# Kernel tuning notes

Measured on AMD Instinct MI355X. Metric: run time of the kernel, lower is better.

Reference implementation:

```python
import jax, jax.numpy as jnp
import numpy as np
import math

DIFF = True   # params['diff'] -> kind='random_walk'
SHIFT = 0.0   # params['shift']
MIN_WINDOW = 10
EPS = 1e-6


def _window_sizes(T):
    ws = []
    cur = math.log10(MIN_WINDOW)
    end = math.log10(T - 1)
    while cur < end:
        w = int(10 ** cur)
        if MIN_WINDOW <= w <= T - 1:
            ws.append(w)
        cur += 0.25
    if T not in ws:
        ws.append(T)
    return sorted(set(ws))


def _hurst_random_walk(x):
    B, T = x.shape
    ws = _window_sizes(T)  # static python list (shapes are static)
    rs_list = []
    for w in ws:
        n = T // w
        seg = x[:, : n * w].reshape(B, n, w)            # (B, n, w)
        d = seg[..., 1:] - seg[..., :-1]                # (B, n, w-1)
        mean_inc = (seg[..., -1] - seg[..., 0]) / (w - 1)
        dev = d - mean_inc[..., None]
        Z = jnp.cumsum(dev, axis=-1)                    # rescaled-range scan
        R = jnp.max(Z, axis=-1) - jnp.min(Z, axis=-1)   # (B, n)
        S = jnp.std(d, axis=-1, ddof=1)                 # unbiased std
        rs_list.append(jnp.mean(R / (S + EPS), axis=-1))
    RS = jnp.stack(rs_list, axis=1)                     # (B, K)
    X = jnp.log10(jnp.asarray(ws, dtype=x.dtype) + EPS) # (K,)
    Y = jnp.log10(RS + EPS)
    Xc = X - jnp.mean(X)
    denom = jnp.sum(Xc * Xc)
    H = jnp.sum((Y - jnp.mean(Y, axis=1, keepdims=True)) * Xc, axis=1) / (denom + EPS)
    H = jnp.where(jnp.isfinite(H), H, jnp.asarray(1.0, x.dtype))
    return H


def setup_inputs() -> dict:
    key = jax.random.key(0)
    x = jax.random.normal(key, (8192, 4096), dtype=jnp.float32)
    return {"x": x}


def reference(x):
    H = _hurst_random_walk(x)
    return (H + SHIFT)[:, None]  # (B, 1)
```

## Files before the change

kernel.cpp:

```cpp
#include <hip/hip_runtime.h>
#include <math.h>
#include <utility>

#define TLEN 4096
#define NW   12
#define BLOCK 256
#define EPSF 1e-6f

typedef float v2f __attribute__((ext_vector_type(2)));

__device__ const float XC_TAB[NW] = {
    -1.3608041f, -1.1303552f, -0.8694424f, -0.6126161f,
    -0.3608041f, -0.1128308f,  0.1388830f,  0.3889322f,
     0.6391959f,  0.8891277f,  1.1391578f,  1.2515558f };
__device__ const float INVN_TAB[NW] = {
    1.0f/409.0f, 1.0f/240.0f, 1.0f/132.0f, 1.0f/73.0f,
    1.0f/40.0f,  1.0f/23.0f,  1.0f/12.0f,  1.0f/7.0f,
    0.25f, 0.5f, 1.0f, 1.0f };
#define INV_DEN 0.11577579f
#define LOG10_2 0.30102999566f

__device__ __forceinline__ float max3f(float a, float b, float c) {
    float r; asm("v_max3_f32 %0, %1, %2, %3" : "=v"(r) : "v"(a), "v"(b), "v"(c)); return r;
}
__device__ __forceinline__ float min3f(float a, float b, float c) {
    float r; asm("v_min3_f32 %0, %1, %2, %3" : "=v"(r) : "v"(a), "v"(b), "v"(c)); return r;
}
__device__ __forceinline__ v2f pk_fma(v2f a, v2f b, v2f c) {
    v2f d; asm("v_pk_fma_f32 %0, %1, %2, %3" : "=v"(d) : "v"(a), "v"(b), "v"(c)); return d;
}
__device__ __forceinline__ v2f pk_add(v2f a, v2f b) {
    v2f d; asm("v_pk_add_f32 %0, %1, %2" : "=v"(d) : "v"(a), "v"(b)); return d;
}

__device__ __forceinline__ float wave_reduce_sum(float v) {
    #pragma unroll
    for (int o = 32; o > 0; o >>= 1) v += __shfl_xor(v, o, 64);
    return v;
}
template<int G>
__device__ __forceinline__ float reduce_leaders(float v) {
    #pragma unroll
    for (int o = G; o < 64; o <<= 1) v += __shfl_xor(v, o, 64);
    return v;
}

template<int FLO, int FHI>
__device__ __forceinline__ float seg_rs2(const float* __restrict__ row,
                                         const float* __restrict__ P4,
                                         int b, int W, float m, float invwm2,
                                         float mx, float mn) {
    float plo = P4[b >> 2];
    if constexpr (FLO > 0) {
        const int k0 = b - FLO;
        #pragma unroll
        for (int t = 0; t < FLO; ++t) {
            float d = row[k0 + t + 1] - row[k0 + t];
            plo = fmaf(d, d, plo);
        }
    }
    const int e = b + W - 1;
    float phi = P4[e >> 2];
    if constexpr (FHI > 0) {
        const int k0 = e - FHI;
        #pragma unroll
        for (int t = 0; t < FHI; ++t) {
            float d = row[k0 + t + 1] - row[k0 + t];
            phi = fmaf(d, d, phi);
        }
    }
    float ss  = phi - plo;
    float var = fmaf(-(float)(W - 1) * m, m, ss) * invwm2;
    float S   = __builtin_amdgcn_sqrtf(fmaxf(var, 0.0f));
    return (mx - mn) * __builtin_amdgcn_rcpf(S + EPSF);
}

template<int LO, int HI, int JB>
__device__ __forceinline__ void chunk_fold(const float4 q, float nm, float& mx, float& mn) {
    if constexpr (LO <= HI) {
        constexpr int NV = HI - LO + 1;
        float v[NV];
        #pragma unroll
        for (int r = 0; r < NV; ++r)
            v[r] = fmaf((float)(JB + LO + r), nm, (&q.x)[LO + r]);
        if constexpr (NV == 1) { mx = fmaxf(mx, v[0]); mn = fminf(mn, v[0]); }
        else if constexpr (NV == 2) { mx = max3f(mx, v[0], v[1]); mn = min3f(mn, v[0], v[1]); }
        else if constexpr (NV == 3) { mx = fmaxf(mx, max3f(v[0], v[1], v[2]));
                                      mn = fminf(mn, min3f(v[0], v[1], v[2])); }
        else { mx = max3f(max3f(mx, v[0], v[1]), v[2], v[3]);
               mn = min3f(min3f(mn, v[0], v[1]), v[2], v[3]); }
    }
}

template<int W, int NSEG, int C>
__device__ __forceinline__ void mchunk_step(const float4* __restrict__ p,
                                            const float (&nm)[NSEG],
                                            float (&mx)[NSEG], float (&mn)[NSEG]) {
    constexpr int E0 = 4 * C;
    constexpr int K0 = E0 / W;
    constexpr int SA = K0 * W;
    constexpr int LOA = (SA == E0) ? 1 : 0;
    constexpr int HIA_ = SA + W - 1 - E0;
    constexpr int HIA = HIA_ < 3 ? HIA_ : 3;
    float4 q = p[C];
    if constexpr (K0 < NSEG)
        chunk_fold<LOA, HIA, E0 - SA>(q, nm[K0], mx[K0], mn[K0]);
    constexpr bool HASB = (K0 + 1 < NSEG) && (SA + W + 1 - E0 <= 3);
    if constexpr (HASB) {
        constexpr int SB = SA + W;
        chunk_fold<SB + 1 - E0, 3, E0 - SB>(q, nm[K0 + 1], mx[K0 + 1], mn[K0 + 1]);
    }
}

template<int W, int NSEG, int... Cs>
__device__ __forceinline__ void mseg_all(const float4* __restrict__ p,
                                         const float (&nm)[NSEG],
                                         float (&mx)[NSEG], float (&mn)[NSEG],
                                         std::integer_sequence<int, Cs...>) {
    (mchunk_step<W, NSEG, Cs>(p, nm, mx, mn), ...);
}

template<int W, int NSEG, int... Ks>
__device__ __forceinline__ float mseg_rs_all(const float* __restrict__ row,
                                             const float* __restrict__ P4, int b,
                                             const float (&m)[NSEG],
                                             const float (&mx)[NSEG], const float (&mn)[NSEG],
                                             std::integer_sequence<int, Ks...>) {
    constexpr float invwm2 = 1.0f / (float)(W - 2);
    float acc = 0.0f;
    ((acc += seg_rs2<(W * Ks) & 3, (W * Ks + W - 1) & 3>(
          row, P4, b + Ks * W, W, m[Ks], invwm2, mx[Ks], mn[Ks])), ...);
    return acc;
}

template<int W, int NSEG>
__device__ __forceinline__ float mseg_task_odd(const float* __restrict__ row,
                                               const float* __restrict__ P4, int b) {
    constexpr int NCH = (W * NSEG + 3) / 4;
    const float4* p = (const float4*)(row + b);
    float nm[NSEG], m[NSEG], mx[NSEG], mn[NSEG];
    #pragma unroll
    for (int k = 0; k < NSEG; ++k) {
        float a0 = row[b + k * W];
        float a1 = row[b + k * W + W - 1];
        m[k] = (a1 - a0) * (1.0f / (float)(W - 1));
        nm[k] = -m[k];
        mx[k] = -INFINITY; mn[k] = INFINITY;
    }
    mseg_all<W, NSEG>(p, nm, mx, mn, std::make_integer_sequence<int, NCH>{});
    return mseg_rs_all<W, NSEG>(row, P4, b, m, mx, mn,
                                std::make_integer_sequence<int, NSEG>{});
}

template<int W, int A, int G>
__device__ __forceinline__ void seg_strided_pk(const float* __restrict__ row, int b, int lane,
                                               float nm, float& mx, float& mn) {
    constexpr int NCH  = (A + W - 1) / 4 + 1;
    constexpr int HIL  = (A + W - 1) & 3;
    constexpr int MAIN_END = (HIL == 3) ? NCH : NCH - 1;
    constexpr int NFULL = MAIN_END - 1;
    constexpr int FULL  = NFULL / G;
    constexpr int REM   = NFULL % G;
    constexpr int NB    = FULL + (REM > 0 ? 1 : 0);
    const float4* p  = (const float4*)(row + (b - A));
    const float4* pl = p + (1 + lane);
    float4 qs[NB > 0 ? NB : 1];
    #pragma unroll
    for (int i = 0; i < FULL; ++i) qs[i] = pl[i * G];
    if constexpr (REM > 0) { if (lane < REM) qs[FULL] = pl[FULL * G]; }
    mx = -INFINITY; mn = INFINITY;
    v2f jc; jc.x = (float)(4 * (1 + lane) - A); jc.y = jc.x + 1.0f;
    const v2f nm2   = {nm, nm};
    const v2f nm2x2 = {nm + nm, nm + nm};
    const v2f step  = {(float)(4 * G), (float)(4 * G)};
    #pragma unroll
    for (int i = 0; i < FULL; ++i) {
        float4 q = qs[i];
        v2f q01 = {q.x, q.y}, q23 = {q.z, q.w};
        v2f t01 = pk_fma(jc, nm2, q01);
        v2f t23 = pk_fma(jc, nm2, pk_add(q23, nm2x2));
        mx = max3f(max3f(mx, t01.x, t01.y), t23.x, t23.y);
        mn = min3f(min3f(mn, t01.x, t01.y), t23.x, t23.y);
        jc = pk_add(jc, step);
    }
    if constexpr (REM > 0) {
        if (lane < REM) {
            float4 q = qs[FULL];
            v2f q01 = {q.x, q.y}, q23 = {q.z, q.w};
            v2f t01 = pk_fma(jc, nm2, q01);
            v2f t23 = pk_fma(jc, nm2, pk_add(q23, nm2x2));
            mx = max3f(max3f(mx, t01.x, t01.y), t23.x, t23.y);
            mn = min3f(min3f(mn, t01.x, t01.y), t23.x, t23.y);
        }
    }
    if constexpr (A < 3) {
        if (lane == 0) chunk_fold<A + 1, 3, -A>(p[0], nm, mx, mn);
    }
    if constexpr (HIL != 3) {
        if (lane == 1) chunk_fold<0, HIL, 4 * (NCH - 1) - A>(p[NCH - 1], nm, mx, mn);
    }
}

template<int W, int A, int G>
__device__ __forceinline__ float group_seg(const float* __restrict__ row,
                                           const float* __restrict__ P4,
                                           int s, int lane) {
    const int b = s * W;
    float a0 = row[b], a1 = row[b + W - 1];
    float m = (a1 - a0) * (1.0f / (float)(W - 1));
    float nm = -m;
    float mx, mn;
    seg_strided_pk<W, A, G>(row, b, lane, nm, mx, mn);
    #pragma unroll
    for (int o = G / 2; o > 0; o >>= 1) {
        mx = fmaxf(mx, __shfl_xor(mx, o, G));
        mn = fminf(mn, __shfl_xor(mn, o, G));
    }
    float r = seg_rs2<A, (A + W - 1) & 3>(
        row, P4, b, W, m, 1.0f / (float)(W - 2), mx, mn);
    return (lane == 0) ? r : 0.0f;
}

__device__ __forceinline__ float w10_seg10(const float (&v)[10], float ss) {
    const float m = (v[9] - v[0]) * (1.0f / 9.0f), nm = -m;
    float x1 = fmaf(1.0f, nm, v[1]);
    float x2 = fmaf(2.0f, nm, v[2]);
    float x3 = fmaf(3.0f, nm, v[3]);
    float x4 = fmaf(4.0f, nm, v[4]);
    float x5 = fmaf(5.0f, nm, v[5]);
    float x6 = fmaf(6.0f, nm, v[6]);
    float x7 = fmaf(7.0f, nm, v[7]);
    float x8 = fmaf(8.0f, nm, v[8]);
    float x9 = fmaf(9.0f, nm, v[9]);
    float mx = max3f(x1, x2, x3);
    mx = max3f(mx, x4, x5); mx = max3f(mx, x6, x7); mx = max3f(mx, x8, x9);
    float mn = min3f(x1, x2, x3);
    mn = min3f(mn, x4, x5); mn = min3f(mn, x6, x7); mn = min3f(mn, x8, x9);
    float var = fmaf(-9.0f * m, m, ss) * 0.125f;
    float S = __builtin_amdgcn_sqrtf(fmaxf(var, 0.0f));
    return (mx - mn) * __builtin_amdgcn_rcpf(S + EPSF);
}

__global__ __launch_bounds__(BLOCK, 7) void hurst_kernel(const float* __restrict__ x,
                                                         float* __restrict__ out) {
    __shared__ __align__(16) float row[TLEN];
    __shared__ __align__(16) float P4[TLEN / 4];
    __shared__ float rs_sum[NW];
    __shared__ float wred[8];
    __shared__ float wredB[24];

    const int tid = threadIdx.x;
    const int r = blockIdx.x;
    const int w = tid >> 6, l = tid & 63;

    const float4* src = (const float4*)(x + (size_t)r * TLEN);
    float4* dst = (float4*)row;
    #pragma unroll
    for (int i = 0; i < TLEN / 4 / BLOCK; ++i)
        dst[tid + i * BLOCK] = src[tid + i * BLOCK];
    if (tid < NW) rs_sum[tid] = 0.0f;
    __syncthreads();

    {
        float lp1 = 0.0f, lp2 = 0.0f, lp3 = 0.0f, lp4 = 0.0f;
        float total = 0.0f;
        float contrib = 0.0f;
        if (tid < 205) {
            const int b = tid * 20;
            const float4* p = (const float4*)(row + b);
            float4 q0 = p[0], q1 = p[1], q2 = p[2];
            float v[12] = {q0.x,q0.y,q0.z,q0.w, q1.x,q1.y,q1.z,q1.w,
                           q2.x,q2.y,q2.z,q2.w};
            float c = 0.0f, s9 = 0.0f;
            #pragma unroll
            for (int j = 0; j < 10; ++j) {
                if (j == 4) lp1 = c;
                if (j == 8) lp2 = c;
                if (j == 9) s9 = c;
                float d = v[j + 1] - v[j];
                c = fmaf(d, d, c);
            }
            {
                float a1[10] = {v[0],v[1],v[2],v[3],v[4],v[5],v[6],v[7],v[8],v[9]};
                contrib = w10_seg10(a1, s9);
            }
            const float s10 = c;
            const float v10 = v[10], v11 = v[11];
            float d10 = v11 - v10;
            c = fmaf(d10, d10, c);
            if (tid < 204) {
                float4 q3 = p[3], q4 = p[4];
                float u[8] = {q3.x,q3.y,q3.z,q3.w, q4.x,q4.y,q4.z,q4.w};
                float vlast = row[b + 20];
                float d11 = u[0] - v11;
                c = fmaf(d11, d11, c);
                lp3 = c;
                float s19 = 0.0f;
                #pragma unroll
                for (int j = 12; j < 20; ++j) {
                    if (j == 16) lp4 = c;
                    if (j == 19) s19 = c;
                    float nxt = (j + 1 < 20) ? u[j - 11] : vlast;
                    float d = nxt - u[j - 12];
                    c = fmaf(d, d, c);
                }
                float a2[10] = {v10, v11, u[0],u[1],u[2],u[3],u[4],u[5],u[6],u[7]};
                contrib += w10_seg10(a2, s19 - s10);
                total = c;
            } else {
                float4 q3 = p[3];
                float d11 = q3.x - v11;
                c = fmaf(d11, d11, c);
                lp3 = c;
                float d12 = q3.y - q3.x; c = fmaf(d12, d12, c);
                float d13 = q3.z - q3.y; c = fmaf(d13, d13, c);
                float d14 = q3.w - q3.z; c = fmaf(d14, d14, c);
                total = c;
            }
        }
        float incl = total;
        #pragma unroll
        for (int o = 1; o < 64; o <<= 1) {
            float u = __shfl_up(incl, o, 64);
            if (l >= o) incl += u;
        }
        if (l == 63) wred[w] = incl;
        float a = wave_reduce_sum(contrib);
        if (l == 0) atomicAdd(&rs_sum[0], a);
        __syncthreads();
        float off = incl - total;
        #pragma unroll
        for (int w2 = 0; w2 < 4; ++w2)
            if (w2 < w) off += wred[w2];
        if (tid < 204) {
            const int h = tid * 5;
            P4[h]     = off;
            P4[h + 1] = off + lp1;
            P4[h + 2] = off + lp2;
            P4[h + 3] = off + lp3;
            P4[h + 4] = off + lp4;
        } else if (tid == 204) {
            P4[1020] = off;
            P4[1021] = off + lp1;
            P4[1022] = off + lp2;
            P4[1023] = off + lp3;
        }
        __syncthreads();
    }


    {
        float a = group_seg<56, 0, 4>(row, P4, tid >> 2, tid & 3);
        a = reduce_leaders<4>(a);
        if (l == 0) atomicAdd(&rs_sum[3], a);
    }
    {
        float a = group_seg<100, 0, 8>(row, P4, tid >> 3, tid & 7);
        a = reduce_leaders<8>(a);
        if (l == 0) atomicAdd(&rs_sum[4], a);
    }
    {
        const int g4 = (tid >> 4) & 3, gl16 = tid & 15;
        float a = 0.0f;
        if (w == 0) {
            a = group_seg<177, 0, 16>(row, P4, 4 * g4, gl16);
            if (g4 < 2) a += group_seg<177, 0, 16>(row, P4, 4 * (g4 + 4), gl16);
        } else if (w == 1) {
            a = group_seg<177, 1, 16>(row, P4, 4 * g4 + 1, gl16);
            if (g4 < 2) a += group_seg<177, 1, 16>(row, P4, 4 * (g4 + 4) + 1, gl16);
        } else if (w == 2) {
            a = group_seg<177, 2, 16>(row, P4, 4 * g4 + 2, gl16);
            if (g4 < 2) a += group_seg<177, 2, 16>(row, P4, 4 * (g4 + 4) + 2, gl16);
        } else {
            a = group_seg<177, 3, 16>(row, P4, 4 * g4 + 3, gl16);
            if (g4 < 1) a += group_seg<177, 3, 16>(row, P4, 4 * (g4 + 4) + 3, gl16);
        }
        a = reduce_leaders<16>(a);
        if (l == 0) atomicAdd(&rs_sum[5], a);
    }

    if (w == 0) {
        float a = (l < 60) ? mseg_task_odd<17, 4>(row, P4, l * 68) : 0.0f;
        a = wave_reduce_sum(a);
        if (l == 0) atomicAdd(&rs_sum[1], a);
        float c1 = group_seg<316, 0, 16>(row, P4, 8 + ((l >> 4) & 3), l & 15);
        c1 = reduce_leaders<16>(c1);
        if (l == 0) atomicAdd(&rs_sum[6], c1);
    } else if (w == 1) {
        float a = (l < 33) ? mseg_task_odd<31, 4>(row, P4, l * 124) : 0.0f;
        a = wave_reduce_sum(a);
        if (l == 0) atomicAdd(&rs_sum[2], a);
    } else if (w == 2) {
        float c2 = group_seg<100, 0, 8>(row, P4, 32 + (l >> 3), l & 7);
        c2 = reduce_leaders<8>(c2);
        if (l == 0) atomicAdd(&rs_sum[4], c2);
        float c3 = ((l >> 2) < 9) ? group_seg<56, 0, 4>(row, P4, 64 + (l >> 2), l & 3) : 0.0f;
        c3 = reduce_leaders<4>(c3);
        if (l == 0) atomicAdd(&rs_sum[3], c3);
        float c4 = group_seg<562, 2, 32>(row, P4, 1 + 2 * (l >> 5), l & 31);
        c4 = reduce_leaders<32>(c4);
        if (l == 0) atomicAdd(&rs_sum[7], c4);
        float c5 = group_seg<1000, 0, 32>(row, P4, l >> 5, l & 31);
        c5 = reduce_leaders<32>(c5);
        if (l == 0) atomicAdd(&rs_sum[8], c5);
        float c6 = group_seg<316, 0, 16>(row, P4, 4 + ((l >> 4) & 3), l & 15);
        c6 = reduce_leaders<16>(c6);
        if (l == 0) atomicAdd(&rs_sum[6], c6);
    } else {
        float c1 = group_seg<562, 0, 32>(row, P4, 2 * (l >> 5), l & 31);
        c1 += group_seg<562, 0, 32>(row, P4, 4 + 2 * (l >> 5), l & 31);
        float c2 = (l < 32) ? group_seg<562, 2, 32>(row, P4, 5, l & 31) : 0.0f;
        c1 += c2;
        c1 = reduce_leaders<32>(c1);
        if (l == 0) atomicAdd(&rs_sum[7], c1);
        float c3 = group_seg<1000, 0, 32>(row, P4, 2 + (l >> 5), l & 31);
        c3 = reduce_leaders<32>(c3);
        if (l == 0) atomicAdd(&rs_sum[8], c3);
        float c4 = group_seg<316, 0, 16>(row, P4, (l >> 4) & 3, l & 15);
        c4 = reduce_leaders<16>(c4);
        if (l == 0) atomicAdd(&rs_sum[6], c4);
    }

    {
        const int half = tid >> 7, hl = tid & 127;
        const int b17 = half ? 1778 : 0;
        float m17 = (row[b17 + 1777] - row[b17]) * (1.0f / 1777.0f);
        float mx17, mn17;
        if (half == 0) seg_strided_pk<1778, 0, 128>(row, 0,    hl, -m17, mx17, mn17);
        else           seg_strided_pk<1778, 2, 128>(row, 1778, hl, -m17, mx17, mn17);

        float m31 = (row[3161] - row[0]) * (1.0f / 3161.0f);
        float mx31, mn31;
        seg_strided_pk<3162, 0, 256>(row, 0, tid, -m31, mx31, mn31);

        float m40 = (row[4095] - row[0]) * (1.0f / 4095.0f);
        float mx40, mn40;
        seg_strided_pk<4096, 0, 256>(row, 0, tid, -m40, mx40, mn40);

        #pragma unroll
        for (int o = 32; o > 0; o >>= 1) {
            mx17 = fmaxf(mx17, __shfl_xor(mx17, o, 64));
            mn17 = fminf(mn17, __shfl_xor(mn17, o, 64));
            mx31 = fmaxf(mx31, __shfl_xor(mx31, o, 64));
            mn31 = fminf(mn31, __shfl_xor(mn31, o, 64));
            mx40 = fmaxf(mx40, __shfl_xor(mx40, o, 64));
            mn40 = fminf(mn40, __shfl_xor(mn40, o, 64));
        }
        if (l == 0) {
            float* wb = wredB + w * 6;
            wb[0] = mx17; wb[1] = mn17;
            wb[2] = mx31; wb[3] = mn31;
            wb[4] = mx40; wb[5] = mn40;
        }
        __syncthreads();
        if (tid == 0) {
            float MX = fmaxf(wredB[0], wredB[6]);
            float MN = fminf(wredB[1], wredB[7]);
            atomicAdd(&rs_sum[9],
                      seg_rs2<0, 1>(row, P4, 0, 1778, m17, 1.0f / 1776.0f, MX, MN));
        } else if (tid == 128) {
            float MX = fmaxf(wredB[12], wredB[18]);
            float MN = fminf(wredB[13], wredB[19]);
            atomicAdd(&rs_sum[9],
                      seg_rs2<2, 3>(row, P4, 1778, 1778, m17, 1.0f / 1776.0f, MX, MN));
        } else if (tid == 64) {
            float MX = fmaxf(fmaxf(wredB[2], wredB[8]),  fmaxf(wredB[14], wredB[20]));
            float MN = fminf(fminf(wredB[3], wredB[9]),  fminf(wredB[15], wredB[21]));
            atomicAdd(&rs_sum[10],
                      seg_rs2<0, 1>(row, P4, 0, 3162, m31, 1.0f / 3160.0f, MX, MN));
        } else if (tid == 192) {
            float MX = fmaxf(fmaxf(wredB[4], wredB[10]), fmaxf(wredB[16], wredB[22]));
            float MN = fminf(fminf(wredB[5], wredB[11]), fminf(wredB[17], wredB[23]));
            atomicAdd(&rs_sum[11],
                      seg_rs2<0, 3>(row, P4, 0, 4096, m40, 1.0f / 4094.0f, MX, MN));
        }
        __syncthreads();
    }

    if (tid < 64) {
        float t = 0.0f;
        if (tid < NW) {
            float rs = fmaf(rs_sum[tid], INVN_TAB[tid], EPSF);
            t = __builtin_amdgcn_logf(rs) * (LOG10_2) * XC_TAB[tid];
        }
        t = wave_reduce_sum(t);
        if (tid == 0) {
            float h = t * INV_DEN;
            if (!isfinite(h)) h = 1.0f;
            out[r] = h;
        }
    }
}

extern "C" void kernel_launch(void* const* d_in, const int* in_sizes, int n_in,
                              void* d_out, int out_size, void* d_ws, size_t ws_size,
                              hipStream_t stream) {
    const float* x = (const float*)d_in[0];
    float* out = (float*)d_out;
    const int B = out_size;
    hipLaunchKernelGGL(hurst_kernel, dim3(B), dim3(BLOCK), 0, stream, x, out);
}
```

Baseline: 84.75 us.

## Spread w=17 and w=31 segments across all waves and rebalance per-wave work

Replaces the per-lane multi-segment tasks for window sizes 17 and 31, which ran on waves 0 and 1 only, with single-segment-per-lane functions. Segment s is now assigned to wave s mod 4, so each wave handles one compile-time alignment. The remaining window-size tasks are then redistributed across the four waves to even out their load. This targets the imbalance that left waves 0 and 1 as the critical path, at the cost of more reductions and atomics per wave and more template instantiations, which may raise code size and register use.

```diff
diff --git a/kernel.cpp b/kernel.cpp
--- a/kernel.cpp
+++ b/kernel.cpp
@@ -92,64 +92,84 @@
     }
 }
 
-template<int W, int NSEG, int C>
-__device__ __forceinline__ void mchunk_step(const float4* __restrict__ p,
-                                            const float (&nm)[NSEG],
-                                            float (&mx)[NSEG], float (&mn)[NSEG]) {
-    constexpr int E0 = 4 * C;
-    constexpr int K0 = E0 / W;
-    constexpr int SA = K0 * W;
-    constexpr int LOA = (SA == E0) ? 1 : 0;
-    constexpr int HIA_ = SA + W - 1 - E0;
-    constexpr int HIA = HIA_ < 3 ? HIA_ : 3;
-    float4 q = p[C];
-    if constexpr (K0 < NSEG)
-        chunk_fold<LOA, HIA, E0 - SA>(q, nm[K0], mx[K0], mn[K0]);
-    constexpr bool HASB = (K0 + 1 < NSEG) && (SA + W + 1 - E0 <= 3);
-    if constexpr (HASB) {
-        constexpr int SB = SA + W;
-        chunk_fold<SB + 1 - E0, 3, E0 - SB>(q, nm[K0 + 1], mx[K0 + 1], mn[K0 + 1]);
-    }
-}
-
-template<int W, int NSEG, int... Cs>
-__device__ __forceinline__ void mseg_all(const float4* __restrict__ p,
-                                         const float (&nm)[NSEG],
-                                         float (&mx)[NSEG], float (&mn)[NSEG],
-                                         std::integer_sequence<int, Cs...>) {
-    (mchunk_step<W, NSEG, Cs>(p, nm, mx, mn), ...);
-}
-
-template<int W, int NSEG, int... Ks>
-__device__ __forceinline__ float mseg_rs_all(const float* __restrict__ row,
-                                             const float* __restrict__ P4, int b,
-                                             const float (&m)[NSEG],
-                                             const float (&mx)[NSEG], const float (&mn)[NSEG],
-                                             std::integer_sequence<int, Ks...>) {
-    constexpr float invwm2 = 1.0f / (float)(W - 2);
-    float acc = 0.0f;
-    ((acc += seg_rs2<(W * Ks) & 3, (W * Ks + W - 1) & 3>(
-          row, P4, b + Ks * W, W, m[Ks], invwm2, mx[Ks], mn[Ks])), ...);
-    return acc;
-}
-
-template<int W, int NSEG>
-__device__ __forceinline__ float mseg_task_odd(const float* __restrict__ row,
-                                               const float* __restrict__ P4, int b) {
-    constexpr int NCH = (W * NSEG + 3) / 4;
-    const float4* p = (const float4*)(row + b);
-    float nm[NSEG], m[NSEG], mx[NSEG], mn[NSEG];
-    #pragma unroll
-    for (int k = 0; k < NSEG; ++k) {
-        float a0 = row[b + k * W];
-        float a1 = row[b + k * W + W - 1];
-        m[k] = (a1 - a0) * (1.0f / (float)(W - 1));
-        nm[k] = -m[k];
-        mx[k] = -INFINITY; mn[k] = INFINITY;
-    }
-    mseg_all<W, NSEG>(p, nm, mx, mn, std::make_integer_sequence<int, NCH>{});
-    return mseg_rs_all<W, NSEG>(row, P4, b, m, mx, mn,
-                                std::make_integer_sequence<int, NSEG>{});
+template<int A>
+__device__ __forceinline__ float w17_seg(const float* __restrict__ row,
+                                         const float* __restrict__ P4, int s) {
+    const int b = 17 * s;
+    const int h = b >> 2;
+    const float4* p = (const float4*)(row + b - A);
+    float4 q0 = p[0], q1 = p[1], q2 = p[2], q3 = p[3], q4 = p[4];
+    const float a0  = (&q0.x)[A];
+    const float a16 = (&q4.x)[A];
+    const float m = (a16 - a0) * (1.0f / 16.0f), nm = -m;
+    float mx = -INFINITY, mn = INFINITY;
+    chunk_fold<A + 1, 3, -A>(q0, nm, mx, mn);
+    chunk_fold<0, 3, 4 - A>(q1, nm, mx, mn);
+    chunk_fold<0, 3, 8 - A>(q2, nm, mx, mn);
+    chunk_fold<0, 3, 12 - A>(q3, nm, mx, mn);
+    chunk_fold<0, A, 16 - A>(q4, nm, mx, mn);
+    float plo = P4[h];
+    float phi = P4[h + 4];
+    #pragma unroll
+    for (int t = 0; t < A; ++t) {
+        float d0 = (&q0.x)[t + 1] - (&q0.x)[t];
+        plo = fmaf(d0, d0, plo);
+        float d1 = (&q4.x)[t + 1] - (&q4.x)[t];
+        phi = fmaf(d1, d1, phi);
+    }
+    float ss = phi - plo;
+    float var = fmaf(-16.0f * m, m, ss) * (1.0f / 15.0f);
+    float S = __builtin_amdgcn_sqrtf(fmaxf(var, 0.0f));
+    return (mx - mn) * __builtin_amdgcn_rcpf(S + EPSF);
+}
+
+template<int A>
+__device__ __forceinline__ float w31_seg(const float* __restrict__ row,
+                                         const float* __restrict__ P4, int s) {
+    const int b = 31 * s;
+    const int h = b >> 2;
+    const float4* p = (const float4*)(row + b - A);
+    float4 q0 = p[0], q1 = p[1], q2 = p[2], q3 = p[3];
+    float4 q4 = p[4], q5 = p[5], q6 = p[6], q7 = p[7];
+    float4 q8 = {};
+    float a30;
+    if constexpr (A >= 2) { q8 = p[8]; a30 = (&q8.x)[A - 2]; }
+    else                  { a30 = (&q7.x)[A + 2]; }
+    const float a0 = (&q0.x)[A];
+    const float m = (a30 - a0) * (1.0f / 30.0f), nm = -m;
+    float mx = -INFINITY, mn = INFINITY;
+    chunk_fold<A + 1, 3, -A>(q0, nm, mx, mn);
+    chunk_fold<0, 3, 4 - A>(q1, nm, mx, mn);
+    chunk_fold<0, 3, 8 - A>(q2, nm, mx, mn);
+    chunk_fold<0, 3, 12 - A>(q3, nm, mx, mn);
+    chunk_fold<0, 3, 16 - A>(q4, nm, mx, mn);
+    chunk_fold<0, 3, 20 - A>(q5, nm, mx, mn);
+    chunk_fold<0, 3, 24 - A>(q6, nm, mx, mn);
+    chunk_fold<0, (A + 2 < 3 ? A + 2 : 3), 28 - A>(q7, nm, mx, mn);
+    if constexpr (A >= 2)
+        chunk_fold<0, A - 2, 32 - A>(q8, nm, mx, mn);
+    float plo = P4[h];
+    #pragma unroll
+    for (int t = 0; t < A; ++t) {
+        float d0 = (&q0.x)[t + 1] - (&q0.x)[t];
+        plo = fmaf(d0, d0, plo);
+    }
+    constexpr int HOF = (A + 30) >> 2;
+    float phi = P4[h + HOF];
+    if constexpr (A == 0) {
+        float d0 = q7.y - q7.x; phi = fmaf(d0, d0, phi);
+        float d1 = q7.z - q7.y; phi = fmaf(d1, d1, phi);
+    } else if constexpr (A == 1) {
+        float d0 = q7.y - q7.x; phi = fmaf(d0, d0, phi);
+        float d1 = q7.z - q7.y; phi = fmaf(d1, d1, phi);
+        float d2 = q7.w - q7.z; phi = fmaf(d2, d2, phi);
+    } else if constexpr (A == 3) {
+        float d0 = q8.y - q8.x; phi = fmaf(d0, d0, phi);
+    }
+    float ss = phi - plo;
+    float var = fmaf(-30.0f * m, m, ss) * (1.0f / 29.0f);
+    float S = __builtin_amdgcn_sqrtf(fmaxf(var, 0.0f));
+    return (mx - mn) * __builtin_amdgcn_rcpf(S + EPSF);
 }
 
 template<int W, int A, int G>
@@ -350,6 +370,30 @@
 
 
     {
+        float a = 0.0f;
+        if (l < 60) {
+            const int s = 4 * l + w;
+            if (w == 0)      a = w17_seg<0>(row, P4, s);
+            else if (w == 1) a = w17_seg<1>(row, P4, s);
+            else if (w == 2) a = w17_seg<2>(row, P4, s);
+            else             a = w17_seg<3>(row, P4, s);
+        }
+        a = wave_reduce_sum(a);
+        if (l == 0) atomicAdd(&rs_sum[1], a);
+    }
+    {
+        float a = 0.0f;
+        if (l < 33) {
+            const int s = 4 * l + w;
+            if (w == 0)      a = w31_seg<0>(row, P4, s);
+            else if (w == 1) a = w31_seg<3>(row, P4, s);
+            else if (w == 2) a = w31_seg<2>(row, P4, s);
+            else             a = w31_seg<1>(row, P4, s);
+        }
+        a = wave_reduce_sum(a);
+        if (l == 0) atomicAdd(&rs_sum[2], a);
+    }
+    {
         float a = group_seg<56, 0, 4>(row, P4, tid >> 2, tid & 3);
         a = reduce_leaders<4>(a);
         if (l == 0) atomicAdd(&rs_sum[3], a);
@@ -380,40 +424,32 @@
     }
 
     if (w == 0) {
-        float a = (l < 60) ? mseg_task_odd<17, 4>(row, P4, l * 68) : 0.0f;
-        a = wave_reduce_sum(a);
-        if (l == 0) atomicAdd(&rs_sum[1], a);
+        float c2 = group_seg<100, 0, 8>(row, P4, 32 + (l >> 3), l & 7);
+        c2 = reduce_leaders<8>(c2);
+        if (l == 0) atomicAdd(&rs_sum[4], c2);
         float c1 = group_seg<316, 0, 16>(row, P4, 8 + ((l >> 4) & 3), l & 15);
         c1 = reduce_leaders<16>(c1);
         if (l == 0) atomicAdd(&rs_sum[6], c1);
     } else if (w == 1) {
-        float a = (l < 33) ? mseg_task_odd<31, 4>(row, P4, l * 124) : 0.0f;
-        a = wave_reduce_sum(a);
-        if (l == 0) atomicAdd(&rs_sum[2], a);
+        float c1 = group_seg<562, 0, 32>(row, P4, 2 * (l >> 5), l & 31);
+        c1 += group_seg<562, 0, 32>(row, P4, 4 + 2 * (l >> 5), l & 31);
+        c1 = reduce_leaders<32>(c1);
+        if (l == 0) atomicAdd(&rs_sum[7], c1);
+        float c6 = group_seg<316, 0, 16>(row, P4, 4 + ((l >> 4) & 3), l & 15);
+        c6 = reduce_leaders<16>(c6);
+        if (l == 0) atomicAdd(&rs_sum[6], c6);
     } else if (w == 2) {
-        float c2 = group_seg<100, 0, 8>(row, P4, 32 + (l >> 3), l & 7);
-        c2 = reduce_leaders<8>(c2);
-        if (l == 0) atomicAdd(&rs_sum[4], c2);
+        float c4 = group_seg<562, 2, 32>(row, P4, 1 + 2 * (l >> 5), l & 31);
+        float c5 = (l < 32) ? group_seg<562, 2, 32>(row, P4, 5, l & 31) : 0.0f;
+        c4 += c5;
+        c4 = reduce_leaders<32>(c4);
+        if (l == 0) atomicAdd(&rs_sum[7], c4);
         float c3 = ((l >> 2) < 9) ? group_seg<56, 0, 4>(row, P4, 64 + (l >> 2), l & 3) : 0.0f;
         c3 = reduce_leaders<4>(c3);
         if (l == 0) atomicAdd(&rs_sum[3], c3);
-        float c4 = group_seg<562, 2, 32>(row, P4, 1 + 2 * (l >> 5), l & 31);
-        c4 = reduce_leaders<32>(c4);
-        if (l == 0) atomicAdd(&rs_sum[7], c4);
-        float c5 = group_seg<1000, 0, 32>(row, P4, l >> 5, l & 31);
-        c5 = reduce_leaders<32>(c5);
-        if (l == 0) atomicAdd(&rs_sum[8], c5);
-        float c6 = group_seg<316, 0, 16>(row, P4, 4 + ((l >> 4) & 3), l & 15);
-        c6 = reduce_leaders<16>(c6);
-        if (l == 0) atomicAdd(&rs_sum[6], c6);
     } else {
-        float c1 = group_seg<562, 0, 32>(row, P4, 2 * (l >> 5), l & 31);
-        c1 += group_seg<562, 0, 32>(row, P4, 4 + 2 * (l >> 5), l & 31);
-        float c2 = (l < 32) ? group_seg<562, 2, 32>(row, P4, 5, l & 31) : 0.0f;
-        c1 += c2;
-        c1 = reduce_leaders<32>(c1);
-        if (l == 0) atomicAdd(&rs_sum[7], c1);
-        float c3 = group_seg<1000, 0, 32>(row, P4, 2 + (l >> 5), l & 31);
+        float c3 = group_seg<1000, 0, 32>(row, P4, l >> 5, l & 31);
+        c3 += group_seg<1000, 0, 32>(row, P4, 2 + (l >> 5), l & 31);
         c3 = reduce_leaders<32>(c3);
         if (l == 0) atomicAdd(&rs_sum[8], c3);
         float c4 = group_seg<316, 0, 16>(row, P4, (l >> 4) & 3, l & 15);
```

After: 88.17 us. +4.0%, slower.
